# Optimization experiments

Hardware: AMD Instinct MI355X
Metric: run time of the kernel (lower is better)

## Reference

```python
import jax, jax.numpy as jnp
import numpy as np
from jax import lax

# Shared Conv2d [1,1] + BN + ReLU is represented as a per-point affine (BN folded
# into conv weight/bias at eval) followed by ReLU, matching inference-mode math.

B, N1, N2, K = 8, 8192, 2048, 8
C1, C2 = 64, 128
MLP0, MLP1, MLP2 = 128, 128, 128  # mlp=[128,128], mlp2=[128]


def setup_inputs() -> dict:
    key = jax.random.key(0)
    ks = jax.random.split(key, 10)
    sc = lambda fan_in: 1.0 / np.sqrt(fan_in)
    return {
        "xyz1": jax.random.normal(ks[0], (B, N1, 3), jnp.float32),
        "xyz2": jax.random.normal(ks[1], (B, N2, 3), jnp.float32),
        "feat1": jax.random.normal(ks[2], (B, N1, C1), jnp.float32),
        "feat2": jax.random.normal(ks[3], (B, N2, C2), jnp.float32),
        "W0": jax.random.normal(ks[4], (C2 + 3, MLP0), jnp.float32) * sc(C2 + 3),
        "b0": jnp.zeros((MLP0,), jnp.float32),
        "W1": jax.random.normal(ks[5], (MLP0, MLP1), jnp.float32) * sc(MLP0),
        "b1": jnp.zeros((MLP1,), jnp.float32),
        "W2": jax.random.normal(ks[6], (MLP1 + C1, MLP2), jnp.float32) * sc(MLP1 + C1),
        "b2": jnp.zeros((MLP2,), jnp.float32),
    }


def _knn_idx(xyz1, xyz2, k):
    # squared distances (B, N1, N2); top-k nearest in xyz2 for each xyz1 point
    d2 = jnp.sum((xyz1[:, :, None, :] - xyz2[:, None, :, :]) ** 2, axis=-1)
    _, idx = lax.top_k(-d2, k)  # (B, N1, K)
    return idx


def _gather(src, idx):
    # src: (B, N2, C), idx: (B, N1, K) -> (B, N1, K, C)
    return jax.vmap(lambda s, i: s[i])(src, idx)


def reference(xyz1, xyz2, feat1, feat2, W0, b0, W1, b1, W2, b2):
    idx = _knn_idx(xyz1, xyz2, K)
    xyz2_g = _gather(xyz2, idx)            # (B, N1, K, 3)
    feat2_g = _gather(feat2, idx)          # (B, N1, K, C2)
    xyz_diff = xyz2_g - xyz1[:, :, None, :]
    net = jnp.concatenate([feat2_g, xyz_diff], axis=-1)  # (B, N1, K, C2+3)
    net = jax.nn.relu(net @ W0 + b0)
    net = jax.nn.relu(net @ W1 + b1)       # (B, N1, K, MLP1)
    pooled = jnp.max(net, axis=2)          # max pooling over neighbors
    cat = jnp.concatenate([pooled, feat1], axis=-1)      # (B, N1, MLP1+C1)
    out = jax.nn.relu(cat @ W2 + b2)       # (B, N1, MLP2)
    return out
```

## Files before the change

### kernel.cpp

```cpp
#include <hip/hip_runtime.h>
#include <hip/hip_bf16.h>

constexpr int B_  = 8;
constexpr int N1_ = 8192;
constexpr int N2_ = 2048;
constexpr int K_  = 8;

typedef short bf16x8 __attribute__((ext_vector_type(8)));
typedef float f32x4  __attribute__((ext_vector_type(4)));

__device__ __forceinline__ short f2b(float x) {
    __hip_bfloat16 h = __float2bfloat16(x);
    return *reinterpret_cast<short*>(&h);
}

#define CASU(a, b) { const unsigned _lo = (a) < (b) ? (a) : (b); \
                     const unsigned _hi = (a) < (b) ? (b) : (a); \
                     (a) = _lo; (b) = _hi; }

__global__ __launch_bounds__(256) void prep_feat2(const float* __restrict__ feat2,
                                                  short* __restrict__ feat2b) {
    const int i = blockIdx.x * 256 + threadIdx.x;
    const float4 v = ((const float4*)feat2)[i];
    uint2 o;
    o.x = (unsigned short)f2b(v.x) | ((unsigned)(unsigned short)f2b(v.y) << 16);
    o.y = (unsigned short)f2b(v.z) | ((unsigned)(unsigned short)f2b(v.w) << 16);
    ((uint2*)feat2b)[i] = o;
}

__global__ __launch_bounds__(256) void prep_weights(
    const float* __restrict__ W0, const float* __restrict__ W1,
    const float* __restrict__ W2, const float* __restrict__ xyz2,
    short* __restrict__ W0T, short* __restrict__ W1T, short* __restrict__ W2T,
    float4* __restrict__ xpack) {
    int i = blockIdx.x * 256 + threadIdx.x;
    if (i < 128 * 160) {
        const int n = i / 160, k = i % 160;
        W0T[i] = (k < 131) ? f2b(W0[k * 128 + n]) : (short)0;
        return;
    }
    i -= 128 * 160;
    if (i < 128 * 128) {
        const int n = i >> 7, k = i & 127;
        W1T[i] = f2b(W1[k * 128 + n]);
        return;
    }
    i -= 128 * 128;
    if (i < 128 * 192) {
        const int n = i / 192, k = i % 192;
        W2T[i] = f2b(W2[k * 128 + n]);
        return;
    }
    i -= 128 * 192;
    xpack[i] = make_float4(xyz2[i * 3 + 0], xyz2[i * 3 + 1], xyz2[i * 3 + 2], 0.f);
}

constexpr int LCAP = 76;

__global__ __launch_bounds__(256) void knn_lazy(const float* __restrict__ xyz1,
                                                const float4* __restrict__ xpack,
                                                int* __restrict__ idx) {
    __shared__ __align__(16) unsigned short sMem[78 * 256];
    float* sD = (float*)sMem;
    int*   sI = (int*)sMem + 64 * 33;

    const int b = blockIdx.y;
    const int lane = threadIdx.x & 63;
    const int s = threadIdx.x >> 6;
    const int tid = threadIdx.x;
    const int n = blockIdx.x * 64 + lane;

    const float* q = xyz1 + ((size_t)b * N1_ + n) * 3;
    const float qx = q[0], qy = q[1], qz = q[2];
    const float4* P = xpack + (size_t)b * N2_ + s * 512;

    unsigned bd[K_];
#pragma unroll
    for (int t = 0; t < K_; ++t) bd[t] = __float_as_uint(3.0e38f);
    int cnt = 0;

    for (int j0 = 0; j0 < 512; j0 += 8) {
        unsigned xu[8];
#pragma unroll
        for (int u = 0; u < 8; ++u) {
#pragma clang fp contract(off)
            const float4 p = P[j0 + u];
            const float dx = qx - p.x;
            const float dy = qy - p.y;
            const float dz = qz - p.z;
            const float dx2 = dx * dx;
            const float dy2 = dy * dy;
            const float dz2 = dz * dz;
            xu[u] = __float_as_uint((dx2 + dy2) + dz2);
        }
        const unsigned thr = bd[K_ - 1];
#pragma unroll
        for (int u = 0; u < 8; ++u) {
            const bool acc = xu[u] < thr;
            const int capped = cnt < LCAP ? cnt : LCAP;
            const int slot = acc ? capped : (LCAP + 1);
            sMem[slot * 256 + tid] = (unsigned short)(j0 + u);
            cnt += acc ? 1 : 0;
        }
        CASU(xu[0], xu[1]); CASU(xu[2], xu[3]); CASU(xu[4], xu[5]); CASU(xu[6], xu[7]);
        CASU(xu[0], xu[2]); CASU(xu[1], xu[3]); CASU(xu[4], xu[6]); CASU(xu[5], xu[7]);
        CASU(xu[1], xu[2]); CASU(xu[5], xu[6]); CASU(xu[0], xu[4]); CASU(xu[3], xu[7]);
        CASU(xu[1], xu[5]); CASU(xu[2], xu[6]);
        CASU(xu[1], xu[4]); CASU(xu[3], xu[6]);
        CASU(xu[2], xu[4]); CASU(xu[3], xu[5]);
        CASU(xu[3], xu[4]);
        unsigned t0 = bd[0] < xu[7] ? bd[0] : xu[7];
        unsigned t1 = bd[1] < xu[6] ? bd[1] : xu[6];
        unsigned t2 = bd[2] < xu[5] ? bd[2] : xu[5];
        unsigned t3 = bd[3] < xu[4] ? bd[3] : xu[4];
        unsigned t4 = bd[4] < xu[3] ? bd[4] : xu[3];
        unsigned t5 = bd[5] < xu[2] ? bd[5] : xu[2];
        unsigned t6 = bd[6] < xu[1] ? bd[6] : xu[1];
        unsigned t7 = bd[7] < xu[0] ? bd[7] : xu[0];
        CASU(t0, t4); CASU(t1, t5); CASU(t2, t6); CASU(t3, t7);
        CASU(t0, t2); CASU(t1, t3); CASU(t4, t6); CASU(t5, t7);
        CASU(t0, t1); CASU(t2, t3); CASU(t4, t5); CASU(t6, t7);
        bd[0] = t0; bd[1] = t1; bd[2] = t2; bd[3] = t3;
        bd[4] = t4; bd[5] = t5; bd[6] = t6; bd[7] = t7;
    }

    float rd[K_];
    int   ri[K_];
#pragma unroll
    for (int t = 0; t < K_; ++t) { rd[t] = 3.0e38f; ri[t] = 0; }
    const int m = cnt < LCAP ? cnt : LCAP;
    for (int t = 0;; ++t) {
        const bool act = t < m;
        if (!__any(act)) break;
        if (act) {
#pragma clang fp contract(off)
            const int jl = sMem[t * 256 + tid];
            const float4 p = P[jl];
            const float dx = qx - p.x;
            const float dy = qy - p.y;
            const float dz = qz - p.z;
            const float dx2 = dx * dx;
            const float dy2 = dy * dy;
            const float dz2 = dz * dz;
            const float d2 = (dx2 + dy2) + dz2;
            if (d2 < rd[K_ - 1]) {
                rd[K_ - 1] = d2; ri[K_ - 1] = s * 512 + jl;
#pragma unroll
                for (int t2 = K_ - 1; t2 >= 1; --t2) {
                    if (rd[t2] < rd[t2 - 1]) {
                        float td = rd[t2]; rd[t2] = rd[t2 - 1]; rd[t2 - 1] = td;
                        int   ti = ri[t2]; ri[t2] = ri[t2 - 1]; ri[t2 - 1] = ti;
                    }
                }
            }
        }
    }

    if (__any(cnt > LCAP)) {
        if (cnt > LCAP) {
#pragma unroll
            for (int t = 0; t < K_; ++t) { rd[t] = 3.0e38f; ri[t] = 0; }
            for (int j = 0; j < 512; ++j) {
#pragma clang fp contract(off)
                const float4 p = P[j];
                const float dx = qx - p.x;
                const float dy = qy - p.y;
                const float dz = qz - p.z;
                const float dx2 = dx * dx;
                const float dy2 = dy * dy;
                const float dz2 = dz * dz;
                const float d2 = (dx2 + dy2) + dz2;
                if (d2 < rd[K_ - 1]) {
                    rd[K_ - 1] = d2; ri[K_ - 1] = s * 512 + j;
#pragma unroll
                    for (int t2 = K_ - 1; t2 >= 1; --t2) {
                        if (rd[t2] < rd[t2 - 1]) {
                            float td = rd[t2]; rd[t2] = rd[t2 - 1]; rd[t2 - 1] = td;
                            int   ti = ri[t2]; ri[t2] = ri[t2 - 1]; ri[t2 - 1] = ti;
                        }
                    }
                }
            }
        }
    }

    __syncthreads();
#pragma unroll
    for (int t = 0; t < K_; ++t) {
        sD[lane * 33 + s * 8 + t] = rd[t];
        sI[lane * 33 + s * 8 + t] = ri[t];
    }
    __syncthreads();

    if (tid < 64) {
        const int qq = tid;
        int h[4] = {0, 0, 0, 0};
        const int base = (b * N1_ + n) * K_;
#pragma unroll
        for (int t = 0; t < K_; ++t) {
            float best = 3.1e38f;
            int   bidx = 0, bs = 0;
#pragma unroll
            for (int ss = 0; ss < 4; ++ss) {
                if (h[ss] < 8) {
                    const float d = sD[qq * 33 + ss * 8 + h[ss]];
                    if (d < best) { best = d; bidx = sI[qq * 33 + ss * 8 + h[ss]]; bs = ss; }
                }
            }
            h[bs]++;
            idx[base + t] = bidx;
        }
    }
}

__global__ __launch_bounds__(256) void fused_mfma(
    const float* __restrict__ xyz1, const float* __restrict__ xyz2,
    const float* __restrict__ feat1,
    const float* __restrict__ b0, const float* __restrict__ b1,
    const float* __restrict__ b2,
    const short* __restrict__ feat2b, const short* __restrict__ W0T,
    const short* __restrict__ W1T, const short* __restrict__ W2T,
    const int* __restrict__ idx, float* __restrict__ out) {
    __shared__ __align__(16) short sA[128 * 168];
    __shared__ __align__(16) short sCat[16 * 200];

    const int b = blockIdx.y;
    const int n0 = blockIdx.x * 16;
    const int tid = threadIdx.x;

    {
        const int row = tid >> 1, half = tid & 1;
        const int p = row >> 3, kk = row & 7;
        const int n = n0 + p;
        const int j = idx[((size_t)b * N1_ + n) * K_ + kk];
        const uint4* src = (const uint4*)(feat2b + ((size_t)(b * N2_ + j)) * 128 + half * 64);
        uint4* dst = (uint4*)(sA + row * 168 + half * 64);
#pragma unroll
        for (int t = 0; t < 8; ++t) dst[t] = src[t];
        uint4* pad = (uint4*)(sA + row * 168 + 128 + half * 16);
        if (half == 0) {
            const float dx = xyz2[((size_t)b * N2_ + j) * 3 + 0] - xyz1[((size_t)b * N1_ + n) * 3 + 0];
            const float dy = xyz2[((size_t)b * N2_ + j) * 3 + 1] - xyz1[((size_t)b * N1_ + n) * 3 + 1];
            const float dz = xyz2[((size_t)b * N2_ + j) * 3 + 2] - xyz1[((size_t)b * N1_ + n) * 3 + 2];
            uint4 v;
            v.x = (unsigned short)f2b(dx) | ((unsigned)(unsigned short)f2b(dy) << 16);
            v.y = (unsigned short)f2b(dz);
            v.z = 0; v.w = 0;
            pad[0] = v;
            pad[1] = make_uint4(0, 0, 0, 0);
        } else {
            pad[0] = make_uint4(0, 0, 0, 0);
            pad[1] = make_uint4(0, 0, 0, 0);
        }
    }
    {
#pragma unroll
        for (int u = 0; u < 4; ++u) {
            const int e = tid * 4 + u;
            const int p = e >> 6, c = e & 63;
            sCat[p * 200 + 128 + c] = f2b(feat1[((size_t)b * N1_ + n0 + p) * 64 + c]);
        }
    }
    __syncthreads();

    const int wave = tid >> 6, lane = tid & 63;
    const int q = lane >> 4, l15 = lane & 15;
    const int mBase = (wave & 1) * 64, nBase = (wave >> 1) * 64;

    const f32x4 zero4 = {0.f, 0.f, 0.f, 0.f};

    f32x4 acc[4][4];
#pragma unroll
    for (int mt = 0; mt < 4; ++mt)
#pragma unroll
        for (int nt = 0; nt < 4; ++nt) acc[mt][nt] = zero4;

    for (int ks = 0; ks < 5; ++ks) {
        bf16x8 af[4], bf[4];
#pragma unroll
        for (int mt = 0; mt < 4; ++mt)
            af[mt] = *(const bf16x8*)(sA + (mBase + mt * 16 + l15) * 168 + ks * 32 + q * 8);
#pragma unroll
        for (int nt = 0; nt < 4; ++nt)
            bf[nt] = *(const bf16x8*)(W0T + (nBase + nt * 16 + l15) * 160 + ks * 32 + q * 8);
#pragma unroll
        for (int mt = 0; mt < 4; ++mt)
#pragma unroll
            for (int nt = 0; nt < 4; ++nt)
                acc[mt][nt] = __builtin_amdgcn_mfma_f32_16x16x32_bf16(af[mt], bf[nt], acc[mt][nt], 0, 0, 0);
    }

    float b0v[4];
#pragma unroll
    for (int nt = 0; nt < 4; ++nt) b0v[nt] = b0[nBase + nt * 16 + l15];
    __syncthreads();
#pragma unroll
    for (int mt = 0; mt < 4; ++mt)
#pragma unroll
        for (int nt = 0; nt < 4; ++nt)
#pragma unroll
            for (int r = 0; r < 4; ++r) {
                const int row = mBase + mt * 16 + q * 4 + r;
                const int col = nBase + nt * 16 + l15;
                sA[row * 136 + col] = f2b(fmaxf(acc[mt][nt][r] + b0v[nt], 0.0f));
            }
    __syncthreads();

    f32x4 acc2[4][4];
#pragma unroll
    for (int mt = 0; mt < 4; ++mt)
#pragma unroll
        for (int nt = 0; nt < 4; ++nt) acc2[mt][nt] = zero4;

    for (int ks = 0; ks < 4; ++ks) {
        bf16x8 af[4], bf[4];
#pragma unroll
        for (int mt = 0; mt < 4; ++mt)
            af[mt] = *(const bf16x8*)(sA + (mBase + mt * 16 + l15) * 136 + ks * 32 + q * 8);
#pragma unroll
        for (int nt = 0; nt < 4; ++nt)
            bf[nt] = *(const bf16x8*)(W1T + (nBase + nt * 16 + l15) * 128 + ks * 32 + q * 8);
#pragma unroll
        for (int mt = 0; mt < 4; ++mt)
#pragma unroll
            for (int nt = 0; nt < 4; ++nt)
                acc2[mt][nt] = __builtin_amdgcn_mfma_f32_16x16x32_bf16(af[mt], bf[nt], acc2[mt][nt], 0, 0, 0);
    }

    float b1v[4];
#pragma unroll
    for (int nt = 0; nt < 4; ++nt) b1v[nt] = b1[nBase + nt * 16 + l15];
#pragma unroll
    for (int mt = 0; mt < 4; ++mt)
#pragma unroll
        for (int nt = 0; nt < 4; ++nt) {
            float vm = fmaxf(acc2[mt][nt][0] + b1v[nt], 0.0f);
#pragma unroll
            for (int r = 1; r < 4; ++r) vm = fmaxf(vm, acc2[mt][nt][r] + b1v[nt]);
            const float other = __shfl_xor(vm, 16);
            const float pool = fmaxf(vm, other);
            if ((q & 1) == 0) {
                const int pp = (mBase >> 3) + mt * 2 + (q >> 1);
                sCat[pp * 200 + nBase + nt * 16 + l15] = f2b(pool);
            }
        }
    __syncthreads();

    f32x4 acc3[2];
    acc3[0] = zero4; acc3[1] = zero4;
    const int nB2 = wave * 32;
    for (int ks = 0; ks < 6; ++ks) {
        const bf16x8 a2 = *(const bf16x8*)(sCat + l15 * 200 + ks * 32 + q * 8);
#pragma unroll
        for (int nt = 0; nt < 2; ++nt) {
            const bf16x8 b2f = *(const bf16x8*)(W2T + (nB2 + nt * 16 + l15) * 192 + ks * 32 + q * 8);
            acc3[nt] = __builtin_amdgcn_mfma_f32_16x16x32_bf16(a2, b2f, acc3[nt], 0, 0, 0);
        }
    }
    float b2v[2];
#pragma unroll
    for (int nt = 0; nt < 2; ++nt) b2v[nt] = b2[nB2 + nt * 16 + l15];
#pragma unroll
    for (int nt = 0; nt < 2; ++nt)
#pragma unroll
        for (int r = 0; r < 4; ++r) {
            const int p = q * 4 + r;
            const int col = nB2 + nt * 16 + l15;
            out[((size_t)(b * N1_ + n0 + p)) * 128 + col] = fmaxf(acc3[nt][r] + b2v[nt], 0.0f);
        }
}

extern "C" void kernel_launch(void* const* d_in, const int* in_sizes, int n_in,
                              void* d_out, int out_size, void* d_ws, size_t ws_size,
                              hipStream_t stream) {
    const float* xyz1  = (const float*)d_in[0];
    const float* xyz2  = (const float*)d_in[1];
    const float* feat1 = (const float*)d_in[2];
    const float* feat2 = (const float*)d_in[3];
    const float* W0    = (const float*)d_in[4];
    const float* b0    = (const float*)d_in[5];
    const float* W1    = (const float*)d_in[6];
    const float* b1    = (const float*)d_in[7];
    const float* W2    = (const float*)d_in[8];
    const float* b2    = (const float*)d_in[9];
    float* out = (float*)d_out;

    char* ws = (char*)d_ws;
    int*    idx    = (int*)(ws + 0);
    short*  feat2b = (short*)(ws + 2097152);
    short*  W0T    = (short*)(ws + 6291456);
    short*  W1T    = (short*)(ws + 6332416);
    short*  W2T    = (short*)(ws + 6365184);
    float4* xpack  = (float4*)(ws + 6414336);

    prep_feat2<<<2048, 256, 0, stream>>>(feat2, feat2b);
    prep_weights<<<304, 256, 0, stream>>>(W0, W1, W2, xyz2, W0T, W1T, W2T, xpack);
    knn_lazy<<<dim3(N1_ / 64, B_), 256, 0, stream>>>(xyz1, xpack, idx);
    fused_mfma<<<dim3(N1_ / 16, B_), 256, 0, stream>>>(xyz1, xyz2, feat1, b0, b1, b2,
                                                       feat2b, W0T, W1T, W2T, idx, out);
}
```

Baseline: 326.0 us.

## Replace KNN candidate index list with per-window bitmasks and 8-way split

The KNN kernel no longer writes every candidate index into a capped LDS list with per-element stores. For each 32-point window it builds a 32-bit acceptance mask, stores one word, and in the second pass walks the set bits with ctz to recompute exact distances. This removes the LCAP overflow fallback that rescanned all points. The block now covers 32 queries with 8 segments of 256 points instead of 64 queries with 4 segments of 512, and the final merge is 8-way. Each thread does less serial work and LDS traffic drops, at the cost of a longer final merge and more blocks.

```diff
diff --git a/kernel.cpp b/kernel.cpp
--- a/kernel.cpp
+++ b/kernel.cpp
@@ -55,86 +55,85 @@
     xpack[i] = make_float4(xyz2[i * 3 + 0], xyz2[i * 3 + 1], xyz2[i * 3 + 2], 0.f);
 }
 
-constexpr int LCAP = 76;
-
-__global__ __launch_bounds__(256) void knn_lazy(const float* __restrict__ xyz1,
-                                                const float4* __restrict__ xpack,
-                                                int* __restrict__ idx) {
-    __shared__ __align__(16) unsigned short sMem[78 * 256];
-    float* sD = (float*)sMem;
-    int*   sI = (int*)sMem + 64 * 33;
+__global__ __launch_bounds__(256, 8) void knn_reg(const float* __restrict__ xyz1,
+                                                  const float4* __restrict__ xpack,
+                                                  int* __restrict__ idx) {
+    __shared__ __align__(16) unsigned sBuf[4160];
+    float* sD = (float*)sBuf;
+    int*   sI = (int*)sBuf + 32 * 65;
 
     const int b = blockIdx.y;
-    const int lane = threadIdx.x & 63;
-    const int s = threadIdx.x >> 6;
+    const int qq = threadIdx.x & 31;
+    const int s = threadIdx.x >> 5;
     const int tid = threadIdx.x;
-    const int n = blockIdx.x * 64 + lane;
-
-    const float* q = xyz1 + ((size_t)b * N1_ + n) * 3;
-    const float qx = q[0], qy = q[1], qz = q[2];
-    const float4* P = xpack + (size_t)b * N2_ + s * 512;
+    const int n = blockIdx.x * 32 + qq;
+
+    const float* qp = xyz1 + ((size_t)b * N1_ + n) * 3;
+    const float qx = qp[0], qy = qp[1], qz = qp[2];
+    const float4* P = xpack + (size_t)b * N2_ + s * 256;
 
     unsigned bd[K_];
 #pragma unroll
     for (int t = 0; t < K_; ++t) bd[t] = __float_as_uint(3.0e38f);
-    int cnt = 0;
-
-    for (int j0 = 0; j0 < 512; j0 += 8) {
-        unsigned xu[8];
-#pragma unroll
-        for (int u = 0; u < 8; ++u) {
+
+    for (int w = 0; w < 8; ++w) {
+        unsigned mw = 0;
+#pragma unroll
+        for (int bb = 0; bb < 4; ++bb) {
+            const int j0 = w * 32 + bb * 8;
+            unsigned xu[8];
+#pragma unroll
+            for (int u = 0; u < 8; ++u) {
 #pragma clang fp contract(off)
-            const float4 p = P[j0 + u];
-            const float dx = qx - p.x;
-            const float dy = qy - p.y;
-            const float dz = qz - p.z;
-            const float dx2 = dx * dx;
-            const float dy2 = dy * dy;
-            const float dz2 = dz * dz;
-            xu[u] = __float_as_uint((dx2 + dy2) + dz2);
-        }
-        const unsigned thr = bd[K_ - 1];
-#pragma unroll
-        for (int u = 0; u < 8; ++u) {
-            const bool acc = xu[u] < thr;
-            const int capped = cnt < LCAP ? cnt : LCAP;
-            const int slot = acc ? capped : (LCAP + 1);
-            sMem[slot * 256 + tid] = (unsigned short)(j0 + u);
-            cnt += acc ? 1 : 0;
-        }
-        CASU(xu[0], xu[1]); CASU(xu[2], xu[3]); CASU(xu[4], xu[5]); CASU(xu[6], xu[7]);
-        CASU(xu[0], xu[2]); CASU(xu[1], xu[3]); CASU(xu[4], xu[6]); CASU(xu[5], xu[7]);
-        CASU(xu[1], xu[2]); CASU(xu[5], xu[6]); CASU(xu[0], xu[4]); CASU(xu[3], xu[7]);
-        CASU(xu[1], xu[5]); CASU(xu[2], xu[6]);
-        CASU(xu[1], xu[4]); CASU(xu[3], xu[6]);
-        CASU(xu[2], xu[4]); CASU(xu[3], xu[5]);
-        CASU(xu[3], xu[4]);
-        unsigned t0 = bd[0] < xu[7] ? bd[0] : xu[7];
-        unsigned t1 = bd[1] < xu[6] ? bd[1] : xu[6];
-        unsigned t2 = bd[2] < xu[5] ? bd[2] : xu[5];
-        unsigned t3 = bd[3] < xu[4] ? bd[3] : xu[4];
-        unsigned t4 = bd[4] < xu[3] ? bd[4] : xu[3];
-        unsigned t5 = bd[5] < xu[2] ? bd[5] : xu[2];
-        unsigned t6 = bd[6] < xu[1] ? bd[6] : xu[1];
-        unsigned t7 = bd[7] < xu[0] ? bd[7] : xu[0];
-        CASU(t0, t4); CASU(t1, t5); CASU(t2, t6); CASU(t3, t7);
-        CASU(t0, t2); CASU(t1, t3); CASU(t4, t6); CASU(t5, t7);
-        CASU(t0, t1); CASU(t2, t3); CASU(t4, t5); CASU(t6, t7);
-        bd[0] = t0; bd[1] = t1; bd[2] = t2; bd[3] = t3;
-        bd[4] = t4; bd[5] = t5; bd[6] = t6; bd[7] = t7;
+                const float4 p = P[j0 + u];
+                const float dx = qx - p.x;
+                const float dy = qy - p.y;
+                const float dz = qz - p.z;
+                const float dx2 = dx * dx;
+                const float dy2 = dy * dy;
+                const float dz2 = dz * dz;
+                xu[u] = __float_as_uint((dx2 + dy2) + dz2);
+            }
+            const unsigned thr = bd[K_ - 1];
+            unsigned m8 = 0;
+#pragma unroll
+            for (int u = 0; u < 8; ++u) m8 |= (xu[u] < thr) ? (1u << u) : 0u;
+            mw |= m8 << (bb * 8);
+            CASU(xu[0], xu[1]); CASU(xu[2], xu[3]); CASU(xu[4], xu[5]); CASU(xu[6], xu[7]);
+            CASU(xu[0], xu[2]); CASU(xu[1], xu[3]); CASU(xu[4], xu[6]); CASU(xu[5], xu[7]);
+            CASU(xu[1], xu[2]); CASU(xu[5], xu[6]); CASU(xu[0], xu[4]); CASU(xu[3], xu[7]);
+            CASU(xu[1], xu[5]); CASU(xu[2], xu[6]);
+            CASU(xu[1], xu[4]); CASU(xu[3], xu[6]);
+            CASU(xu[2], xu[4]); CASU(xu[3], xu[5]);
+            CASU(xu[3], xu[4]);
+            unsigned t0 = bd[0] < xu[7] ? bd[0] : xu[7];
+            unsigned t1 = bd[1] < xu[6] ? bd[1] : xu[6];
+            unsigned t2 = bd[2] < xu[5] ? bd[2] : xu[5];
+            unsigned t3 = bd[3] < xu[4] ? bd[3] : xu[4];
+            unsigned t4 = bd[4] < xu[3] ? bd[4] : xu[3];
+            unsigned t5 = bd[5] < xu[2] ? bd[5] : xu[2];
+            unsigned t6 = bd[6] < xu[1] ? bd[6] : xu[1];
+            unsigned t7 = bd[7] < xu[0] ? bd[7] : xu[0];
+            CASU(t0, t4); CASU(t1, t5); CASU(t2, t6); CASU(t3, t7);
+            CASU(t0, t2); CASU(t1, t3); CASU(t4, t6); CASU(t5, t7);
+            CASU(t0, t1); CASU(t2, t3); CASU(t4, t5); CASU(t6, t7);
+            bd[0] = t0; bd[1] = t1; bd[2] = t2; bd[3] = t3;
+            bd[4] = t4; bd[5] = t5; bd[6] = t6; bd[7] = t7;
+        }
+        sBuf[w * 256 + tid] = mw;
     }
 
     float rd[K_];
     int   ri[K_];
 #pragma unroll
     for (int t = 0; t < K_; ++t) { rd[t] = 3.0e38f; ri[t] = 0; }
-    const int m = cnt < LCAP ? cnt : LCAP;
-    for (int t = 0;; ++t) {
-        const bool act = t < m;
-        if (!__any(act)) break;
-        if (act) {
+    for (int w = 0; w < 8; ++w) {
+        unsigned mw = sBuf[w * 256 + tid];
+        while (mw) {
 #pragma clang fp contract(off)
-            const int jl = sMem[t * 256 + tid];
+            const int u = __builtin_ctz(mw);
+            mw &= mw - 1;
+            const int jl = w * 32 + u;
             const float4 p = P[jl];
             const float dx = qx - p.x;
             const float dy = qy - p.y;
@@ -144,7 +143,7 @@
             const float dz2 = dz * dz;
             const float d2 = (dx2 + dy2) + dz2;
             if (d2 < rd[K_ - 1]) {
-                rd[K_ - 1] = d2; ri[K_ - 1] = s * 512 + jl;
+                rd[K_ - 1] = d2; ri[K_ - 1] = s * 256 + jl;
 #pragma unroll
                 for (int t2 = K_ - 1; t2 >= 1; --t2) {
                     if (rd[t2] < rd[t2 - 1]) {
@@ -156,55 +155,27 @@
         }
     }
 
-    if (__any(cnt > LCAP)) {
-        if (cnt > LCAP) {
-#pragma unroll
-            for (int t = 0; t < K_; ++t) { rd[t] = 3.0e38f; ri[t] = 0; }
-            for (int j = 0; j < 512; ++j) {
-#pragma clang fp contract(off)
-                const float4 p = P[j];
-                const float dx = qx - p.x;
-                const float dy = qy - p.y;
-                const float dz = qz - p.z;
-                const float dx2 = dx * dx;
-                const float dy2 = dy * dy;
-                const float dz2 = dz * dz;
-                const float d2 = (dx2 + dy2) + dz2;
-                if (d2 < rd[K_ - 1]) {
-                    rd[K_ - 1] = d2; ri[K_ - 1] = s * 512 + j;
-#pragma unroll
-                    for (int t2 = K_ - 1; t2 >= 1; --t2) {
-                        if (rd[t2] < rd[t2 - 1]) {
-                            float td = rd[t2]; rd[t2] = rd[t2 - 1]; rd[t2 - 1] = td;
-                            int   ti = ri[t2]; ri[t2] = ri[t2 - 1]; ri[t2 - 1] = ti;
-                        }
-                    }
-                }
-            }
-        }
-    }
-
     __syncthreads();
 #pragma unroll
     for (int t = 0; t < K_; ++t) {
-        sD[lane * 33 + s * 8 + t] = rd[t];
-        sI[lane * 33 + s * 8 + t] = ri[t];
-    }
-    __syncthreads();
-
-    if (tid < 64) {
-        const int qq = tid;
-        int h[4] = {0, 0, 0, 0};
-        const int base = (b * N1_ + n) * K_;
+        sD[qq * 65 + s * 8 + t] = rd[t];
+        sI[qq * 65 + s * 8 + t] = ri[t];
+    }
+    __syncthreads();
+
+    if (tid < 32) {
+        const int q = tid;
+        int h[8] = {0, 0, 0, 0, 0, 0, 0, 0};
+        const int base = (b * N1_ + blockIdx.x * 32 + q) * K_;
 #pragma unroll
         for (int t = 0; t < K_; ++t) {
             float best = 3.1e38f;
             int   bidx = 0, bs = 0;
 #pragma unroll
-            for (int ss = 0; ss < 4; ++ss) {
+            for (int ss = 0; ss < 8; ++ss) {
                 if (h[ss] < 8) {
-                    const float d = sD[qq * 33 + ss * 8 + h[ss]];
-                    if (d < best) { best = d; bidx = sI[qq * 33 + ss * 8 + h[ss]]; bs = ss; }
+                    const float d = sD[q * 65 + ss * 8 + h[ss]];
+                    if (d < best) { best = d; bidx = sI[q * 65 + ss * 8 + h[ss]]; bs = ss; }
                 }
             }
             h[bs]++;
@@ -395,7 +366,7 @@
 
     prep_feat2<<<2048, 256, 0, stream>>>(feat2, feat2b);
     prep_weights<<<304, 256, 0, stream>>>(W0, W1, W2, xyz2, W0T, W1T, W2T, xpack);
-    knn_lazy<<<dim3(N1_ / 64, B_), 256, 0, stream>>>(xyz1, xpack, idx);
+    knn_reg<<<dim3(N1_ / 32, B_), 256, 0, stream>>>(xyz1, xpack, idx);
     fused_mfma<<<dim3(N1_ / 16, B_), 256, 0, stream>>>(xyz1, xyz2, feat1, b0, b1, b2,
                                                        feat2b, W0T, W1T, W2T, idx, out);
 }
```

Measured after the change: 596.0 us. 1.83x slower.
